# Kernel tuning notes

Measured on AMD Instinct MI355X. Metric: run time of the kernel, lower is better.

The kernel has to match this reference:

```python
import jax, jax.numpy as jnp
import numpy as np

NUM_CARDS = 71
NUM_SLOTS = 71
TRUMP_DIM = 7
HIDDEN = [512, 256, 128]
ACTIONS = 9
BATCH = 16384


def setup_inputs() -> dict:
    key = jax.random.key(0)
    ks = jax.random.split(key, 16)
    state_idx = jax.random.randint(ks[0], (BATCH, NUM_SLOTS), 0, NUM_CARDS, dtype=jnp.int32)
    trump_onehot = jax.random.uniform(ks[1], (BATCH, TRUMP_DIM), dtype=jnp.float32)
    legal_mask = jnp.ones((BATCH, ACTIONS), dtype=bool)
    in_dim = NUM_SLOTS * NUM_CARDS + TRUMP_DIM  # 5048
    dims = [in_dim] + HIDDEN
    params = {}
    for i, (d_in, d_out) in enumerate(zip(dims[:-1], dims[1:])):
        params[f"W{i}"] = jax.random.normal(ks[2 + 2 * i], (d_in, d_out), dtype=jnp.float32) * 0.02
        params[f"b{i}"] = jnp.zeros((d_out,), dtype=jnp.float32)
    params["Wp"] = jax.random.normal(ks[10], (dims[-1], ACTIONS), dtype=jnp.float32) * 0.02
    params["bp"] = jnp.zeros((ACTIONS,), dtype=jnp.float32)
    return {"state_idx": state_idx, "trump_onehot": trump_onehot, "legal_mask": legal_mask, **params}


def reference(state_idx, trump_onehot, legal_mask,
              W0, b0, W1, b1, W2, b2, Wp, bp):
    # one-hot encode 71 card slots and flatten: (B, 71*71)
    idx = jnp.clip(state_idx, 0, NUM_CARDS - 1)
    one_hot = jax.nn.one_hot(idx, NUM_CARDS, dtype=jnp.float32)
    flat = one_hot.reshape(one_hot.shape[0], -1)
    x = jnp.concatenate([flat, trump_onehot], axis=1)  # (B, 5048)
    x = jax.nn.relu(x @ W0 + b0)
    x = jax.nn.relu(x @ W1 + b1)
    x = jax.nn.relu(x @ W2 + b2)
    logits = x @ Wp + bp  # (B, 9)
    logits = jnp.where(legal_mask, logits, -jnp.inf)
    return jax.nn.log_softmax(logits, axis=1)
```

## Files before the change

### kernel.cpp

```cpp
#include <hip/hip_runtime.h>
#include <hip/hip_bf16.h>

typedef unsigned int u32;
typedef unsigned short u16;
typedef unsigned char u8;
typedef _Float16 f16;
typedef __attribute__((ext_vector_type(2)))  _Float16 f16x2;
typedef __attribute__((ext_vector_type(8)))  _Float16 f16x8;
typedef __attribute__((ext_vector_type(16))) _Float16 f16x16;
typedef __attribute__((ext_vector_type(4))) float f32x4;

#define NSLOT   71
#define NCARD   71
#define ONEHOT  5041
#define INDIM   5048
#define D0      512
#define D1      256
#define D2      128
#define NACT    9

__device__ __forceinline__ u16 f2h_bits(float x) { f16 h = (f16)x; u16 r; __builtin_memcpy(&r, &h, 2); return r; }

__global__ void prep_kernel(const float* __restrict__ W0, const float* __restrict__ W1,
                            const float* __restrict__ W2,
                            u16* __restrict__ W0h, u16* __restrict__ W1T, u16* __restrict__ W2T) {
    int i = blockIdx.x * 256 + threadIdx.x;
    const int n0 = INDIM * D0;
    const int n1 = D0 * D1;
    const int n2 = D1 * D2;
    if (i < n0) {
        W0h[i] = f2h_bits(W0[i]);
    } else if (i < n0 + n1) {
        int j = i - n0; int n = j >> 9, k = j & 511;
        W1T[j] = f2h_bits(W1[k * D1 + n]);
    } else if (i < n0 + n1 + n2) {
        int j = i - n0 - n1; int n = j >> 8, k = j & 255;
        W2T[j] = f2h_bits(W2[k * D2 + n]);
    }
}

__global__ __launch_bounds__(512)
void layer0_kernel(const int* __restrict__ sidx, const float* __restrict__ trump,
                   const float* __restrict__ b0, const u16* __restrict__ W0h,
                   u16* __restrict__ h0) {
    __shared__ u8 idxl[128 * NSLOT];
    __shared__ float trl[128 * 7];
    const int tid = threadIdx.x;
    const int ct = blockIdx.x & 3;
    const int rbase = (blockIdx.x >> 2) * 128;

    for (int i = tid; i < 128 * NSLOT; i += 512) {
        int v = sidx[rbase * NSLOT + i];
        v = v < 0 ? 0 : (v > NCARD - 1 ? NCARD - 1 : v);
        idxl[i] = (u8)v;
    }
    for (int i = tid; i < 128 * 7; i += 512)
        trl[i] = trump[rbase * 7 + i];
    __syncthreads();

    const int rg = tid >> 3;
    const int cg = tid & 7;
    const int c0 = ct * 128 + cg * 16;
    const u8* ix0 = &idxl[(rg * 2 + 0) * NSLOT];
    const u8* ix1 = &idxl[(rg * 2 + 1) * NSLOT];
    const u16* Wc = W0h + c0;

    f16x16 acc0, acc1;
    {
        f16x16 bias;
        #pragma unroll
        for (int j = 0; j < 16; ++j) bias[j] = (f16)b0[c0 + j];
        acc0 = bias; acc1 = bias;
        #pragma unroll
        for (int t = 0; t < 7; ++t) {
            f16x16 w16 = *(const f16x16*)(Wc + (size_t)(ONEHOT + t) * D0);
            acc0 += w16 * (f16)trl[(rg * 2 + 0) * 7 + t];
            acc1 += w16 * (f16)trl[(rg * 2 + 1) * 7 + t];
        }
    }

#define LD0(s) (*(const f16x16*)(Wc + ((size_t)(s) * NCARD + ix0[(s)]) * D0))
#define LD1(s) (*(const f16x16*)(Wc + ((size_t)(s) * NCARD + ix1[(s)]) * D0))

    f16x16 pa0 = LD0(0), pa1 = LD1(0);
    f16x16 pb0 = LD0(1), pb1 = LD1(1);
    int s = 0;
    for (; s + 3 < NSLOT; s += 2) {
        acc0 += pa0; acc1 += pa1;
        pa0 = LD0(s + 2); pa1 = LD1(s + 2);
        acc0 += pb0; acc1 += pb1;
        pb0 = LD0(s + 3); pb1 = LD1(s + 3);
    }
    acc0 += pa0; acc1 += pa1;
    pa0 = LD0(70); pa1 = LD1(70);
    acc0 += pb0; acc1 += pb1;
    acc0 += pa0; acc1 += pa1;
#undef LD0
#undef LD1

    const f16x16 zero = {};
    f16x16 v0 = __builtin_elementwise_max(acc0, zero);
    f16x16 v1 = __builtin_elementwise_max(acc1, zero);
    uint4* dst0 = (uint4*)(h0 + (size_t)(rbase + rg * 2 + 0) * D0 + c0);
    uint4* dst1 = (uint4*)(h0 + (size_t)(rbase + rg * 2 + 1) * D0 + c0);
    dst0[0] = ((const uint4*)&v0)[0];
    dst0[1] = ((const uint4*)&v0)[1];
    dst1[0] = ((const uint4*)&v1)[0];
    dst1[1] = ((const uint4*)&v1)[1];
}

__global__ __launch_bounds__(512)
void mlp_kernel(const u16* __restrict__ h0, const u16* __restrict__ W1T, const u16* __restrict__ W2T,
                const float* __restrict__ b1, const float* __restrict__ b2,
                const float* __restrict__ Wp, const float* __restrict__ bp,
                const int* __restrict__ legal, float* __restrict__ out) {
    __shared__ u16 Abuf[32 * 520];
    __shared__ u16 h1buf[32 * 264];
    __shared__ u16 h2buf[32 * 136];
    __shared__ float wpb[D2 * NACT + NACT];
    const int tid = threadIdx.x;
    const int r0 = blockIdx.x * 32;

    for (int i = tid; i < 2048; i += 512) {
        int r = i >> 6, g = i & 63;
        uint4 v = *(const uint4*)(h0 + (size_t)(r0 + r) * D0 + g * 8);
        *(uint4*)&Abuf[r * 520 + g * 8] = v;
    }
    for (int i = tid; i < D2 * NACT + NACT; i += 512)
        wpb[i] = (i < D2 * NACT) ? Wp[i] : bp[i - D2 * NACT];
    __syncthreads();

    const int w  = tid >> 6;
    const int l  = tid & 63;
    const int lc = l & 15;
    const int kg = l >> 4;

    {
        const int n0 = w * 32;
        f32x4 a00 = {0.f,0.f,0.f,0.f}, a01 = a00, a10 = a00, a11 = a00;
        for (int kb = 0; kb < D0; kb += 32) {
            f16x8 av0 = *(const f16x8*)&Abuf[lc * 520 + kb + kg * 8];
            f16x8 av1 = *(const f16x8*)&Abuf[(lc + 16) * 520 + kb + kg * 8];
            f16x8 bv0 = *(const f16x8*)(W1T + (size_t)(n0 + lc) * D0 + kb + kg * 8);
            f16x8 bv1 = *(const f16x8*)(W1T + (size_t)(n0 + 16 + lc) * D0 + kb + kg * 8);
            a00 = __builtin_amdgcn_mfma_f32_16x16x32_f16(av0, bv0, a00, 0, 0, 0);
            a01 = __builtin_amdgcn_mfma_f32_16x16x32_f16(av0, bv1, a01, 0, 0, 0);
            a10 = __builtin_amdgcn_mfma_f32_16x16x32_f16(av1, bv0, a10, 0, 0, 0);
            a11 = __builtin_amdgcn_mfma_f32_16x16x32_f16(av1, bv1, a11, 0, 0, 0);
        }
        #pragma unroll
        for (int nb = 0; nb < 2; ++nb) {
            int col = n0 + nb * 16 + lc;
            float bias = b1[col];
            #pragma unroll
            for (int j = 0; j < 4; ++j) {
                f32x4 v0 = nb ? a01 : a00;
                f32x4 v1 = nb ? a11 : a10;
                h1buf[(kg * 4 + j) * 264 + col]        = f2h_bits(fmaxf(v0[j] + bias, 0.f));
                h1buf[(16 + kg * 4 + j) * 264 + col]   = f2h_bits(fmaxf(v1[j] + bias, 0.f));
            }
        }
    }
    __syncthreads();

    {
        const int n0 = w * 16;
        f32x4 c0 = {0.f,0.f,0.f,0.f}, c1 = c0;
        for (int kb = 0; kb < D1; kb += 32) {
            f16x8 av0 = *(const f16x8*)&h1buf[lc * 264 + kb + kg * 8];
            f16x8 av1 = *(const f16x8*)&h1buf[(lc + 16) * 264 + kb + kg * 8];
            f16x8 bv  = *(const f16x8*)(W2T + (size_t)(n0 + lc) * D1 + kb + kg * 8);
            c0 = __builtin_amdgcn_mfma_f32_16x16x32_f16(av0, bv, c0, 0, 0, 0);
            c1 = __builtin_amdgcn_mfma_f32_16x16x32_f16(av1, bv, c1, 0, 0, 0);
        }
        int col = n0 + lc;
        float bias = b2[col];
        #pragma unroll
        for (int j = 0; j < 4; ++j) {
            h2buf[(kg * 4 + j) * 136 + col]      = f2h_bits(fmaxf(c0[j] + bias, 0.f));
            h2buf[(16 + kg * 4 + j) * 136 + col] = f2h_bits(fmaxf(c1[j] + bias, 0.f));
        }
    }
    __syncthreads();

    if (tid < 128) {
        int r = tid >> 2, q = tid & 3;
        float part[NACT];
        #pragma unroll
        for (int a = 0; a < NACT; ++a) part[a] = 0.f;
        int kbase = q * 32;
        #pragma unroll
        for (int kk = 0; kk < 32; kk += 2) {
            u32 pr = *(const u32*)&h2buf[r * 136 + kbase + kk];
            f16x2 hp; __builtin_memcpy(&hp, &pr, 4);
            float x0 = (float)hp.x, x1 = (float)hp.y;
            #pragma unroll
            for (int a = 0; a < NACT; ++a)
                part[a] += x0 * wpb[(kbase + kk) * NACT + a] + x1 * wpb[(kbase + kk + 1) * NACT + a];
        }
        #pragma unroll
        for (int a = 0; a < NACT; ++a) {
            part[a] += __shfl_xor(part[a], 1, 64);
            part[a] += __shfl_xor(part[a], 2, 64);
        }
        if (q == 0) {
            int row = r0 + r;
            const int* mk = legal + (size_t)row * NACT;
            float lg[NACT]; float mx = -INFINITY;
            #pragma unroll
            for (int a = 0; a < NACT; ++a) {
                lg[a] = part[a] + wpb[D2 * NACT + a];
                if (mk[a] != 0 && lg[a] > mx) mx = lg[a];
            }
            float s = 0.f;
            #pragma unroll
            for (int a = 0; a < NACT; ++a) if (mk[a] != 0) s += __expf(lg[a] - mx);
            float lse = mx + __logf(s);
            #pragma unroll
            for (int a = 0; a < NACT; ++a)
                out[(size_t)row * NACT + a] = (mk[a] != 0) ? (lg[a] - lse) : -INFINITY;
        }
    }
}

extern "C" void kernel_launch(void* const* d_in, const int* in_sizes, int n_in,
                              void* d_out, int out_size, void* d_ws, size_t ws_size,
                              hipStream_t stream) {
    const int*   sidx  = (const int*)d_in[0];
    const float* trump = (const float*)d_in[1];
    const int*   legal = (const int*)d_in[2];
    const float* W0 = (const float*)d_in[3];
    const float* b0 = (const float*)d_in[4];
    const float* W1 = (const float*)d_in[5];
    const float* b1 = (const float*)d_in[6];
    const float* W2 = (const float*)d_in[7];
    const float* b2 = (const float*)d_in[8];
    const float* Wp = (const float*)d_in[9];
    const float* bp = (const float*)d_in[10];
    float* out = (float*)d_out;

    u16* W0h  = (u16*)d_ws;
    u16* W1T  = W0h + (size_t)INDIM * D0;
    u16* W2T  = W1T + (size_t)D0 * D1;
    u16* h0   = W2T + (size_t)D1 * D2;

    const int total = INDIM * D0 + D0 * D1 + D1 * D2;
    prep_kernel<<<(total + 255) / 256, 256, 0, stream>>>(W0, W1, W2, W0h, W1T, W2T);
    layer0_kernel<<<512, 512, 0, stream>>>(sidx, trump, b0, W0h, h0);
    mlp_kernel<<<512, 512, 0, stream>>>(h0, W1T, W2T, b1, b2, Wp, bp, legal, out);
}
```

Measured before the change: 82.80 us.

## Fuse layer-0 gather into MLP kernel, keeping h0 in shared memory

Merges the embedding-gather layer-0 kernel into the MLP kernel so each 32-row block computes its h0 directly into LDS instead of writing it to global memory and reading it back. Thread mapping changes to 16 threads per row with 32 columns each, and a sched_barrier is added to separate the gather loads from the accumulation. This removes one launch and the h0 round trip through memory. In exchange it gives up the old 128-row tiling, which reused each row's index data across four column-tile blocks, and it uses about 62 KB of shared memory while asking launch_bounds for 4 blocks per CU, which may not be satisfiable.

```diff
diff --git a/kernel.cpp b/kernel.cpp
--- a/kernel.cpp
+++ b/kernel.cpp
@@ -39,95 +39,86 @@
     }
 }
 
-__global__ __launch_bounds__(512)
-void layer0_kernel(const int* __restrict__ sidx, const float* __restrict__ trump,
-                   const float* __restrict__ b0, const u16* __restrict__ W0h,
-                   u16* __restrict__ h0) {
-    __shared__ u8 idxl[128 * NSLOT];
-    __shared__ float trl[128 * 7];
-    const int tid = threadIdx.x;
-    const int ct = blockIdx.x & 3;
-    const int rbase = (blockIdx.x >> 2) * 128;
-
-    for (int i = tid; i < 128 * NSLOT; i += 512) {
-        int v = sidx[rbase * NSLOT + i];
-        v = v < 0 ? 0 : (v > NCARD - 1 ? NCARD - 1 : v);
-        idxl[i] = (u8)v;
-    }
-    for (int i = tid; i < 128 * 7; i += 512)
-        trl[i] = trump[rbase * 7 + i];
-    __syncthreads();
-
-    const int rg = tid >> 3;
-    const int cg = tid & 7;
-    const int c0 = ct * 128 + cg * 16;
-    const u8* ix0 = &idxl[(rg * 2 + 0) * NSLOT];
-    const u8* ix1 = &idxl[(rg * 2 + 1) * NSLOT];
-    const u16* Wc = W0h + c0;
-
-    f16x16 acc0, acc1;
-    {
-        f16x16 bias;
-        #pragma unroll
-        for (int j = 0; j < 16; ++j) bias[j] = (f16)b0[c0 + j];
-        acc0 = bias; acc1 = bias;
-        #pragma unroll
-        for (int t = 0; t < 7; ++t) {
-            f16x16 w16 = *(const f16x16*)(Wc + (size_t)(ONEHOT + t) * D0);
-            acc0 += w16 * (f16)trl[(rg * 2 + 0) * 7 + t];
-            acc1 += w16 * (f16)trl[(rg * 2 + 1) * 7 + t];
-        }
-    }
-
-#define LD0(s) (*(const f16x16*)(Wc + ((size_t)(s) * NCARD + ix0[(s)]) * D0))
-#define LD1(s) (*(const f16x16*)(Wc + ((size_t)(s) * NCARD + ix1[(s)]) * D0))
-
-    f16x16 pa0 = LD0(0), pa1 = LD1(0);
-    f16x16 pb0 = LD0(1), pb1 = LD1(1);
-    int s = 0;
-    for (; s + 3 < NSLOT; s += 2) {
-        acc0 += pa0; acc1 += pa1;
-        pa0 = LD0(s + 2); pa1 = LD1(s + 2);
-        acc0 += pb0; acc1 += pb1;
-        pb0 = LD0(s + 3); pb1 = LD1(s + 3);
-    }
-    acc0 += pa0; acc1 += pa1;
-    pa0 = LD0(70); pa1 = LD1(70);
-    acc0 += pb0; acc1 += pb1;
-    acc0 += pa0; acc1 += pa1;
-#undef LD0
-#undef LD1
-
-    const f16x16 zero = {};
-    f16x16 v0 = __builtin_elementwise_max(acc0, zero);
-    f16x16 v1 = __builtin_elementwise_max(acc1, zero);
-    uint4* dst0 = (uint4*)(h0 + (size_t)(rbase + rg * 2 + 0) * D0 + c0);
-    uint4* dst1 = (uint4*)(h0 + (size_t)(rbase + rg * 2 + 1) * D0 + c0);
-    dst0[0] = ((const uint4*)&v0)[0];
-    dst0[1] = ((const uint4*)&v0)[1];
-    dst1[0] = ((const uint4*)&v1)[0];
-    dst1[1] = ((const uint4*)&v1)[1];
-}
-
-__global__ __launch_bounds__(512)
-void mlp_kernel(const u16* __restrict__ h0, const u16* __restrict__ W1T, const u16* __restrict__ W2T,
-                const float* __restrict__ b1, const float* __restrict__ b2,
-                const float* __restrict__ Wp, const float* __restrict__ bp,
-                const int* __restrict__ legal, float* __restrict__ out) {
-    __shared__ u16 Abuf[32 * 520];
-    __shared__ u16 h1buf[32 * 264];
-    __shared__ u16 h2buf[32 * 136];
-    __shared__ float wpb[D2 * NACT + NACT];
+__global__ __launch_bounds__(512, 4)
+void fused_kernel(const int* __restrict__ sidx, const float* __restrict__ trump,
+                  const float* __restrict__ b0, const u16* __restrict__ W0h,
+                  const u16* __restrict__ W1T, const u16* __restrict__ W2T,
+                  const float* __restrict__ b1, const float* __restrict__ b2,
+                  const float* __restrict__ Wp, const float* __restrict__ bp,
+                  const int* __restrict__ legal, float* __restrict__ out) {
+    __shared__ __align__(16) u8 smem[63552];
+    u16*  h0buf = (u16*)(smem);
+    u16*  h1buf = (u16*)(smem + 33280);
+    float* wpb  = (float*)(smem + 50176);
+    u16*  h2buf = (u16*)(smem + 54832);
+    u8*   idxl  = smem + 54832;
+    float* trl  = (float*)(smem + 57136);
     const int tid = threadIdx.x;
     const int r0 = blockIdx.x * 32;
 
-    for (int i = tid; i < 2048; i += 512) {
-        int r = i >> 6, g = i & 63;
-        uint4 v = *(const uint4*)(h0 + (size_t)(r0 + r) * D0 + g * 8);
-        *(uint4*)&Abuf[r * 520 + g * 8] = v;
-    }
+    for (int i = tid; i < 32 * NSLOT; i += 512) {
+        int r = i / NSLOT, s = i - r * NSLOT;
+        int v = sidx[r0 * NSLOT + i];
+        v = v < 0 ? 0 : (v > NCARD - 1 ? NCARD - 1 : v);
+        idxl[r * 72 + s] = (u8)v;
+    }
+    for (int i = tid; i < 32 * 7; i += 512)
+        trl[i] = trump[r0 * 7 + i];
     for (int i = tid; i < D2 * NACT + NACT; i += 512)
         wpb[i] = (i < D2 * NACT) ? Wp[i] : bp[i - D2 * NACT];
+    __syncthreads();
+
+    {
+        const int rg = tid >> 4;
+        const int cg = tid & 15;
+        const int c0 = cg * 32;
+        const u8* ixp = &idxl[rg * 72];
+        const u16* Wc = W0h + c0;
+
+        f16x16 acc0, acc1;
+        {
+            #pragma unroll
+            for (int j = 0; j < 16; ++j) { acc0[j] = (f16)b0[c0 + j]; acc1[j] = (f16)b0[c0 + 16 + j]; }
+            #pragma unroll
+            for (int t = 0; t < 7; ++t) {
+                const f16x16* wp = (const f16x16*)(Wc + (size_t)(ONEHOT + t) * D0);
+                f16 tv = (f16)trl[rg * 7 + t];
+                acc0 += wp[0] * tv;
+                acc1 += wp[1] * tv;
+            }
+        }
+
+#define LDP(s) ((const f16x16*)(Wc + (((size_t)((s) * NCARD + ixp[(s)])) << 9)))
+        const f16x16* pa = LDP(0);
+        const f16x16* pb = LDP(1);
+        int s = 0;
+        for (; s + 3 < NSLOT; s += 2) {
+            f16x16 a0 = pa[0], a1 = pa[1];
+            f16x16 b0v = pb[0], b1v = pb[1];
+            const f16x16* na = LDP(s + 2);
+            const f16x16* nb = LDP(s + 3);
+            __builtin_amdgcn_sched_barrier(0);
+            acc0 += a0; acc1 += a1;
+            acc0 += b0v; acc1 += b1v;
+            pa = na; pb = nb;
+        }
+        {
+            const f16x16* pc = LDP(70);
+            acc0 += pa[0]; acc1 += pa[1];
+            acc0 += pb[0]; acc1 += pb[1];
+            acc0 += pc[0]; acc1 += pc[1];
+        }
+#undef LDP
+
+        const f16x16 zero = {};
+        f16x16 v0 = __builtin_elementwise_max(acc0, zero);
+        f16x16 v1 = __builtin_elementwise_max(acc1, zero);
+        uint4* dst = (uint4*)&h0buf[rg * 520 + c0];
+        dst[0] = ((const uint4*)&v0)[0];
+        dst[1] = ((const uint4*)&v0)[1];
+        dst[2] = ((const uint4*)&v1)[0];
+        dst[3] = ((const uint4*)&v1)[1];
+    }
     __syncthreads();
 
     const int w  = tid >> 6;
@@ -139,8 +130,8 @@
         const int n0 = w * 32;
         f32x4 a00 = {0.f,0.f,0.f,0.f}, a01 = a00, a10 = a00, a11 = a00;
         for (int kb = 0; kb < D0; kb += 32) {
-            f16x8 av0 = *(const f16x8*)&Abuf[lc * 520 + kb + kg * 8];
-            f16x8 av1 = *(const f16x8*)&Abuf[(lc + 16) * 520 + kb + kg * 8];
+            f16x8 av0 = *(const f16x8*)&h0buf[lc * 520 + kb + kg * 8];
+            f16x8 av1 = *(const f16x8*)&h0buf[(lc + 16) * 520 + kb + kg * 8];
             f16x8 bv0 = *(const f16x8*)(W1T + (size_t)(n0 + lc) * D0 + kb + kg * 8);
             f16x8 bv1 = *(const f16x8*)(W1T + (size_t)(n0 + 16 + lc) * D0 + kb + kg * 8);
             a00 = __builtin_amdgcn_mfma_f32_16x16x32_f16(av0, bv0, a00, 0, 0, 0);
@@ -242,10 +233,9 @@
     u16* W0h  = (u16*)d_ws;
     u16* W1T  = W0h + (size_t)INDIM * D0;
     u16* W2T  = W1T + (size_t)D0 * D1;
-    u16* h0   = W2T + (size_t)D1 * D2;
 
     const int total = INDIM * D0 + D0 * D1 + D1 * D2;
     prep_kernel<<<(total + 255) / 256, 256, 0, stream>>>(W0, W1, W2, W0h, W1T, W2T);
-    layer0_kernel<<<512, 512, 0, stream>>>(sidx, trump, b0, W0h, h0);
-    mlp_kernel<<<512, 512, 0, stream>>>(h0, W1T, W2T, b1, b2, Wp, bp, legal, out);
+    fused_kernel<<<512, 512, 0, stream>>>(sidx, trump, b0, W0h, W1T, W2T,
+                                          b1, b2, Wp, bp, legal, out);
 }
```

Measured after the change: 111.1 us. +34.2%, slower.
